# Kernel optimization log

Hardware: AMD Instinct MI355X
Metric: run time of the kernel (lower is better)

## Reference

```python
import jax, jax.numpy as jnp
import numpy as np

H = 512          # lstm_hidden_size
NUM_OPS = 8
NUM_NODES = 4
TEMP = 5.0
TANH_C = 2.5
B = 4096
NUM_STEPS = 16   # 8 lstm steps x 2 decisions (node, op)


def setup_inputs() -> dict:
    key = jax.random.key(0)
    ks = jax.random.split(key, 20)
    u = lambda k, s: jax.random.uniform(k, s, jnp.float32, -0.1, 0.1)
    inp = {}
    # embedding: torch default init N(0,1)
    inp["emb"] = jax.random.normal(ks[0], (NUM_OPS + 1, H), jnp.float32)
    # LSTM (single layer), torch gate order i,f,g,o; init U(-0.1,0.1), bias 0
    inp["w_ih"] = u(ks[1], (4 * H, H))
    inp["w_hh"] = u(ks[2], (4 * H, H))
    inp["b_ih"] = jnp.zeros((4 * H,), jnp.float32)
    inp["b_hh"] = jnp.zeros((4 * H,), jnp.float32)
    # node-predecessor decoders: widths 2,3,4,5 (one per intermediate node)
    inp["wn2"] = u(ks[3], (2, H)); inp["bn2"] = jnp.zeros((2,), jnp.float32)
    inp["wn3"] = u(ks[4], (3, H)); inp["bn3"] = jnp.zeros((3,), jnp.float32)
    inp["wn4"] = u(ks[5], (4, H)); inp["bn4"] = jnp.zeros((4,), jnp.float32)
    inp["wn5"] = u(ks[6], (5, H)); inp["bn5"] = jnp.zeros((5,), jnp.float32)
    # op decoders: one [NUM_OPS, H] decoder per intermediate node
    inp["wop"] = u(ks[7], (NUM_NODES, NUM_OPS, H))
    inp["bop"] = jnp.zeros((NUM_NODES, NUM_OPS), jnp.float32)
    # Gumbel noise for multinomial sampling via Gumbel-max (padded to width 8)
    un = jax.random.uniform(ks[8], (NUM_STEPS, B, NUM_OPS), jnp.float32,
                            minval=1e-6, maxval=1.0 - 1e-6)
    inp["gumbel"] = -jnp.log(-jnp.log(un))
    inp["batch_size"] = B
    return inp


def _lstm_step(x, h, c, w_ih, w_hh, b_ih, b_hh):
    gates = x @ w_ih.T + h @ w_hh.T + b_ih + b_hh   # [B, 4H]
    i, f, g, o = jnp.split(gates, 4, axis=-1)
    i = jax.nn.sigmoid(i); f = jax.nn.sigmoid(f)
    g = jnp.tanh(g);       o = jax.nn.sigmoid(o)
    c = f * c + i * g
    h = o * jnp.tanh(c)
    return h, c


def _decide(logits, g):
    # logits: [B, k], g: [B, k] gumbel noise -> sample ~ softmax(logits)
    logp = jax.nn.log_softmax(logits, axis=-1)
    probs = jnp.exp(logp)
    action = jnp.argmax(logits + g, axis=-1)                     # [B]
    sel = jnp.take_along_axis(logp, action[:, None], 1)[:, 0]     # [B]
    ent = -(logp * probs).sum(-1)                                 # [B]
    return action, sel, ent


def reference(emb, w_ih, w_hh, b_ih, b_hh,
              wn2, bn2, wn3, bn3, wn4, bn4, wn5, bn5,
              wop, bop, gumbel, batch_size):
    node_dec = [(wn2, bn2), (wn3, bn3), (wn4, bn4), (wn5, bn5)]
    h = jnp.zeros((batch_size, H), emb.dtype)
    c = jnp.zeros((batch_size, H), emb.dtype)
    inputs = jnp.zeros((batch_size,), jnp.int32)   # initial token 0
    actions, log_probs, entropies = [], [], []
    step = 0
    for i in range(NUM_NODES):
        wn, bn = node_dec[i]
        k = wn.shape[0]
        for _ in range(2):  # two (prev_node, op) edges per node, one lstm step each
            x = emb[inputs]                                   # [B, H]
            h, c = _lstm_step(x, h, c, w_ih, w_hh, b_ih, b_hh)
            # node-predecessor decision: temperature + tanh squashing
            nl = TANH_C * jnp.tanh((h @ wn.T + bn) / TEMP)    # [B, k]
            a, s, e = _decide(nl, gumbel[step, :, :k])
            actions.append(a); log_probs.append(s); entropies.append(e)
            step += 1
            # op decision: temperature only (no tanh in original code)
            ol = (h @ wop[i].T + bop[i]) / TEMP               # [B, NUM_OPS]
            a, s, e = _decide(ol, gumbel[step])
            actions.append(a); log_probs.append(s); entropies.append(e)
            step += 1
            inputs = a  # op action feeds the next lstm step
    return (jnp.stack(actions).astype(jnp.int32),   # [16, B]
            jnp.stack(log_probs),                   # [16, B]
            jnp.stack(entropies))                   # [16, B]
```

## Files before the change

### kernel.cpp

```cpp
#include <hip/hip_runtime.h>


constexpr int Bsz = 4096;
constexpr int Hsz = 512;
constexpr int G4H = 2048;

typedef unsigned short ushort_t;
using short8 = __attribute__((ext_vector_type(8))) short;
using f32x4 = __attribute__((ext_vector_type(4))) float;

__device__ __forceinline__ ushort_t f2bf_hi(float f) {
  unsigned u = __float_as_uint(f);
  u += 0x7FFF + ((u >> 16) & 1);
  return (ushort_t)(u >> 16);
}
__device__ __forceinline__ float bf2f(ushort_t h) {
  return __uint_as_float((unsigned)h << 16);
}
__device__ __forceinline__ float sigf(float x) {
  return 1.0f / (1.0f + expf(-x));
}

__device__ __forceinline__ void glds16(const void* gsrc, void* ldst) {
  __builtin_amdgcn_global_load_lds(
      (const __attribute__((address_space(1))) void*)gsrc,
      (__attribute__((address_space(3))) void*)ldst, 16, 0, 0);
}

__global__ __launch_bounds__(256) void setup_fused(
    const float* __restrict__ emb, const float* __restrict__ w_ih,
    const float* __restrict__ b_ih, const float* __restrict__ b_hh,
    const float* __restrict__ w_hh, float* __restrict__ Eperm,
    ushort_t* __restrict__ Wcat) {
  if (blockIdx.x < 4608) {
    const int lane = threadIdx.x & 63;
    const int wid = (blockIdx.x << 2) + (threadIdx.x >> 6);
    const int t = wid >> 11;
    const int col = wid & 2047;
    const float* er = emb + (size_t)t * Hsz + (lane << 3);
    const float* wr = w_ih + (size_t)col * Hsz + (lane << 3);
    float4 e0 = *(const float4*)(er);
    float4 e1 = *(const float4*)(er + 4);
    float4 w0 = *(const float4*)(wr);
    float4 w1 = *(const float4*)(wr + 4);
    float v = e0.x * w0.x + e0.y * w0.y + e0.z * w0.z + e0.w * w0.w +
              e1.x * w1.x + e1.y * w1.y + e1.z * w1.z + e1.w * w1.w;
#pragma unroll
    for (int off = 32; off > 0; off >>= 1) v += __shfl_xor(v, off, 64);
    if (lane == 0) {
      float val = v + b_ih[col] + b_hh[col];
      Eperm[(size_t)t * G4H + ((col & 511) << 2) + (col >> 9)] = val;
    }
  } else {
    const int b = blockIdx.x - 4608;
    const int ct = b >> 2;
    const int k = ((b & 3) << 8) + threadIdx.x;
    const int j = ct >> 2, g = ct & 3;
    const float* srcrow = w_hh + (size_t)(g * 512 + j) * Hsz;
    ushort_t out;
    if (k < 512) {
      out = f2bf_hi(srcrow[k]);
    } else {
      float x = srcrow[k - 512];
      ushort_t hi = f2bf_hi(x);
      out = f2bf_hi(x - bf2f(hi));
    }
    Wcat[(size_t)ct * 1536 + k] = out;
  }
}

template <int K>
__device__ __forceinline__ void decide_core(
    const float4 hv0, const float4 hv1, const int lane, const int r,
    const float* __restrict__ wn, const float* __restrict__ bn,
    const float* __restrict__ wopi, const float* __restrict__ bopi,
    const float* __restrict__ gum, float* __restrict__ oan,
    float* __restrict__ oao, float* __restrict__ oln, float* __restrict__ olo,
    float* __restrict__ oen, float* __restrict__ oeo,
    int* __restrict__ act_next, const int* __restrict__ cls_prev,
    int* __restrict__ cls_out) {
  float nl[K];
#pragma unroll
  for (int j = 0; j < K; ++j) {
    const float* w = wn + (size_t)j * Hsz;
    float4 w0 = *(const float4*)(w + (lane << 3));
    float4 w1 = *(const float4*)(w + (lane << 3) + 4);
    float v = hv0.x * w0.x + hv0.y * w0.y + hv0.z * w0.z + hv0.w * w0.w +
              hv1.x * w1.x + hv1.y * w1.y + hv1.z * w1.z + hv1.w * w1.w;
#pragma unroll
    for (int off = 32; off > 0; off >>= 1) v += __shfl_xor(v, off, 64);
    nl[j] = 2.5f * tanhf((v + bn[j]) / 5.0f);
  }
  float ol[8];
#pragma unroll
  for (int j = 0; j < 8; ++j) {
    const float* w = wopi + (size_t)j * Hsz;
    float4 w0 = *(const float4*)(w + (lane << 3));
    float4 w1 = *(const float4*)(w + (lane << 3) + 4);
    float v = hv0.x * w0.x + hv0.y * w0.y + hv0.z * w0.z + hv0.w * w0.w +
              hv1.x * w1.x + hv1.y * w1.y + hv1.z * w1.z + hv1.w * w1.w;
#pragma unroll
    for (int off = 32; off > 0; off >>= 1) v += __shfl_xor(v, off, 64);
    ol[j] = (v + bopi[j]) / 5.0f;
  }

  {
    const float* g = gum + (size_t)r * 8;
    float m = nl[0];
#pragma unroll
    for (int j = 1; j < K; ++j) m = fmaxf(m, nl[j]);
    float se = 0.0f;
#pragma unroll
    for (int j = 0; j < K; ++j) se += expf(nl[j] - m);
    float lse = logf(se);
    int a = 0;
    float best = nl[0] + g[0];
#pragma unroll
    for (int j = 1; j < K; ++j) {
      float v = nl[j] + g[j];
      if (v > best) { best = v; a = j; }
    }
    float ent = 0.0f, sel = 0.0f;
#pragma unroll
    for (int j = 0; j < K; ++j) {
      float lp = nl[j] - m - lse;
      ent -= lp * expf(lp);
      if (j == a) sel = lp;
    }
    if (lane == 0) { oan[r] = (float)a; oln[r] = sel; oen[r] = ent; }
  }
  {
    const float* g = gum + (size_t)Bsz * 8 + (size_t)r * 8;
    float m = ol[0];
#pragma unroll
    for (int j = 1; j < 8; ++j) m = fmaxf(m, ol[j]);
    float se = 0.0f;
#pragma unroll
    for (int j = 0; j < 8; ++j) se += expf(ol[j] - m);
    float lse = logf(se);
    int a = 0;
    float best = ol[0] + g[0];
#pragma unroll
    for (int j = 1; j < 8; ++j) {
      float v = ol[j] + g[j];
      if (v > best) { best = v; a = j; }
    }
    float ent = 0.0f, sel = 0.0f;
#pragma unroll
    for (int j = 0; j < 8; ++j) {
      float lp = ol[j] - m - lse;
      ent -= lp * expf(lp);
      if (j == a) sel = lp;
    }
    if (lane == 0) {
      oao[r] = (float)a; olo[r] = sel; oeo[r] = ent;
      act_next[r] = a;
      if (cls_out) cls_out[r] = (cls_prev ? cls_prev[r] * 8 : 0) + a;
    }
  }
}

template <int K>
__device__ __forceinline__ void decide_core_s(
    const float* __restrict__ h8, const int lane, const int r,
    const float* __restrict__ wn, const float* __restrict__ bn,
    const float* __restrict__ wopi, const float* __restrict__ bopi,
    const float* __restrict__ gum, float* __restrict__ oan,
    float* __restrict__ oao, float* __restrict__ oln, float* __restrict__ olo,
    float* __restrict__ oen, float* __restrict__ oeo,
    int* __restrict__ act_next, const int* __restrict__ cls_prev,
    int* __restrict__ cls_out) {
  float nl[K];
#pragma unroll
  for (int j = 0; j < K; ++j) {
    const float* w = wn + (size_t)j * Hsz + lane;
    float v = 0.0f;
#pragma unroll
    for (int kk = 0; kk < 8; ++kk) v = fmaf(h8[kk], w[kk * 64], v);
#pragma unroll
    for (int off = 32; off > 0; off >>= 1) v += __shfl_xor(v, off, 64);
    nl[j] = 2.5f * tanhf((v + bn[j]) / 5.0f);
  }
  float ol[8];
#pragma unroll
  for (int j = 0; j < 8; ++j) {
    const float* w = wopi + (size_t)j * Hsz + lane;
    float v = 0.0f;
#pragma unroll
    for (int kk = 0; kk < 8; ++kk) v = fmaf(h8[kk], w[kk * 64], v);
#pragma unroll
    for (int off = 32; off > 0; off >>= 1) v += __shfl_xor(v, off, 64);
    ol[j] = (v + bopi[j]) / 5.0f;
  }

  {
    const float* g = gum + (size_t)r * 8;
    float m = nl[0];
#pragma unroll
    for (int j = 1; j < K; ++j) m = fmaxf(m, nl[j]);
    float se = 0.0f;
#pragma unroll
    for (int j = 0; j < K; ++j) se += expf(nl[j] - m);
    float lse = logf(se);
    int a = 0;
    float best = nl[0] + g[0];
#pragma unroll
    for (int j = 1; j < K; ++j) {
      float v = nl[j] + g[j];
      if (v > best) { best = v; a = j; }
    }
    float ent = 0.0f, sel = 0.0f;
#pragma unroll
    for (int j = 0; j < K; ++j) {
      float lp = nl[j] - m - lse;
      ent -= lp * expf(lp);
      if (j == a) sel = lp;
    }
    if (lane == 0) { oan[r] = (float)a; oln[r] = sel; oen[r] = ent; }
  }
  {
    const float* g = gum + (size_t)Bsz * 8 + (size_t)r * 8;
    float m = ol[0];
#pragma unroll
    for (int j = 1; j < 8; ++j) m = fmaxf(m, ol[j]);
    float se = 0.0f;
#pragma unroll
    for (int j = 0; j < 8; ++j) se += expf(ol[j] - m);
    float lse = logf(se);
    int a = 0;
    float best = ol[0] + g[0];
#pragma unroll
    for (int j = 1; j < 8; ++j) {
      float v = ol[j] + g[j];
      if (v > best) { best = v; a = j; }
    }
    float ent = 0.0f, sel = 0.0f;
#pragma unroll
    for (int j = 0; j < 8; ++j) {
      float lp = ol[j] - m - lse;
      ent -= lp * expf(lp);
      if (j == a) sel = lp;
    }
    if (lane == 0) {
      oao[r] = (float)a; olo[r] = sel; oeo[r] = ent;
      act_next[r] = a;
      if (cls_out) cls_out[r] = (cls_prev ? cls_prev[r] * 8 : 0) + a;
    }
  }
}

template <int K>
__global__ __launch_bounds__(256) void decide_step(
    const float* __restrict__ h, const float* __restrict__ wn,
    const float* __restrict__ bn, const float* __restrict__ wopi,
    const float* __restrict__ bopi, const float* __restrict__ gum,
    float* __restrict__ oan, float* __restrict__ oao,
    float* __restrict__ oln, float* __restrict__ olo,
    float* __restrict__ oen, float* __restrict__ oeo,
    int* __restrict__ act_next, const int* __restrict__ hidx, int hmode,
    const int* __restrict__ cls_prev, int* __restrict__ cls_out) {
  const int lane = threadIdx.x & 63;
  const int r = (blockIdx.x << 2) + (threadIdx.x >> 6);
  const int idx = (hmode == 1) ? r : hidx[r];
  const float* hr = h + (size_t)idx * Hsz;
  const float4 hv0 = *(const float4*)(hr + (lane << 3));
  const float4 hv1 = *(const float4*)(hr + (lane << 3) + 4);
  decide_core<K>(hv0, hv1, lane, r, wn, bn, wopi, bopi, gum, oan, oao, oln,
                 olo, oen, oeo, act_next, cls_prev, cls_out);
}

__global__ __launch_bounds__(256) void decide0_step(
    const float* __restrict__ Eperm, const float* __restrict__ wn,
    const float* __restrict__ bn, const float* __restrict__ wopi,
    const float* __restrict__ bopi, const float* __restrict__ gum,
    float* __restrict__ oan, float* __restrict__ oao,
    float* __restrict__ oln, float* __restrict__ olo,
    float* __restrict__ oen, float* __restrict__ oeo,
    int* __restrict__ act_next, int* __restrict__ cls_out) {
  const int lane = threadIdx.x & 63;
  const int r = (blockIdx.x << 2) + (threadIdx.x >> 6);
  float h8[8];
#pragma unroll
  for (int kk = 0; kk < 8; ++kk) {
    float4 e = *(const float4*)&Eperm[(size_t)(((lane << 3) + kk) << 2)];
    float ig = sigf(e.x);
    float gg = tanhf(e.z);
    float og = sigf(e.w);
    float cn = ig * gg;
    h8[kk] = og * tanhf(cn);
  }
  float4 hv0 = {h8[0], h8[1], h8[2], h8[3]};
  float4 hv1 = {h8[4], h8[5], h8[6], h8[7]};
  decide_core<2>(hv0, hv1, lane, r, wn, bn, wopi, bopi, gum, oan, oao, oln,
                 olo, oen, oeo, act_next, nullptr, cls_out);
}

__global__ __launch_bounds__(256) void fused_step1(
    const float* __restrict__ Eperm, const float* __restrict__ w_hh,
    float* __restrict__ h2, float* __restrict__ c2) {
  const int lane = threadIdx.x & 63;
  const int j = (blockIdx.x << 2) + (threadIdx.x >> 6);
  float h8[8];
#pragma unroll
  for (int kk = 0; kk < 8; ++kk) {
    float4 e = *(const float4*)&Eperm[(size_t)(((lane << 3) + kk) << 2)];
    h8[kk] = sigf(e.w) * tanhf(sigf(e.x) * tanhf(e.z));
  }
  float v[4];
#pragma unroll
  for (int g = 0; g < 4; ++g) {
    const float* w = w_hh + (size_t)(g * 512 + j) * Hsz + (lane << 3);
    float4 w0 = *(const float4*)(w);
    float4 w1 = *(const float4*)(w + 4);
    v[g] = h8[0] * w0.x + h8[1] * w0.y + h8[2] * w0.z + h8[3] * w0.w +
           h8[4] * w1.x + h8[5] * w1.y + h8[6] * w1.z + h8[7] * w1.w;
  }
#pragma unroll
  for (int off = 32; off > 0; off >>= 1) {
#pragma unroll
    for (int g = 0; g < 4; ++g) v[g] += __shfl_xor(v[g], off, 64);
  }
  float4 e0 = *(const float4*)&Eperm[(size_t)(j << 2)];
  float c1j = sigf(e0.x) * tanhf(e0.z);
  if (lane < 8) {
    const int er = lane;
    float4 e = *(const float4*)&Eperm[(size_t)er * G4H + (j << 2)];
    float ig = sigf(v[0] + e.x);
    float fg = sigf(v[1] + e.y);
    float gg = tanhf(v[2] + e.z);
    float og = sigf(v[3] + e.w);
    float cn = fg * c1j + ig * gg;
    h2[er * Hsz + j] = og * tanhf(cn);
    c2[er * Hsz + j] = cn;
  }
}

__global__ __launch_bounds__(256) void fused_step2(
    const float* __restrict__ Eperm, const float* __restrict__ w_hh,
    const float* __restrict__ h2, const float* __restrict__ c2,
    float* __restrict__ h3, float* __restrict__ c3) {
  const int lane = threadIdx.x & 63;
  const int wid = (blockIdx.x << 2) + (threadIdx.x >> 6);
  const int gq = wid >> 9, j = wid & 511;
  const float* hr = h2 + (size_t)gq * Hsz + (lane << 3);
  float4 a0 = *(const float4*)(hr);
  float4 a1 = *(const float4*)(hr + 4);
  float v[4];
#pragma unroll
  for (int g = 0; g < 4; ++g) {
    const float* w = w_hh + (size_t)(g * 512 + j) * Hsz + (lane << 3);
    float4 w0 = *(const float4*)(w);
    float4 w1 = *(const float4*)(w + 4);
    v[g] = a0.x * w0.x + a0.y * w0.y + a0.z * w0.z + a0.w * w0.w +
           a1.x * w1.x + a1.y * w1.y + a1.z * w1.z + a1.w * w1.w;
  }
#pragma unroll
  for (int off = 32; off > 0; off >>= 1) {
#pragma unroll
    for (int g = 0; g < 4; ++g) v[g] += __shfl_xor(v[g], off, 64);
  }
  float cp = c2[(size_t)gq * Hsz + j];
  if (lane < 8) {
    const int er = lane;
    float4 e = *(const float4*)&Eperm[(size_t)er * G4H + (j << 2)];
    float ig = sigf(v[0] + e.x);
    float fg = sigf(v[1] + e.y);
    float gg = tanhf(v[2] + e.z);
    float og = sigf(v[3] + e.w);
    float cn = fg * cp + ig * gg;
    h3[(size_t)((gq << 3) + er) * Hsz + j] = og * tanhf(cn);
    c3[(size_t)((gq << 3) + er) * Hsz + j] = cn;
  }
}

template <int NRT, int SK>
__global__ __launch_bounds__(256) void gemm64ct_sk(
    const float* __restrict__ A, const float* __restrict__ w_hh,
    float* __restrict__ Gpart) {
  constexpr int LOG = (NRT == 1) ? 0 : (NRT == 2) ? 1 : (NRT == 4) ? 2 : 3;
  constexpr int LDA = 68;
  __shared__ float As[16 * LDA];
  __shared__ float Bs[16 * LDA];
  const int tid = threadIdx.x;
  const int bx = blockIdx.x & 31;
  const int by = (blockIdx.x >> 5) & (NRT - 1);
  const int s = blockIdx.x >> (5 + LOG);
  const int r0 = by * 64, c0 = bx * 64;
  const int tx = tid & 15, ty = tid >> 4;
  const int lr = tid >> 2;
  const int lk = (tid & 3) << 2;
  const int ct = c0 + lr;
  const int brow = (ct & 3) * 512 + (ct >> 2);
  const float* Ar = A + (size_t)(r0 + lr) * Hsz;
  const float* Br = w_hh + (size_t)brow * Hsz;
  float acc[4][4];
#pragma unroll
  for (int i = 0; i < 4; ++i)
#pragma unroll
    for (int j = 0; j < 4; ++j) acc[i][j] = 0.0f;

  const int kBeg = s * (Hsz / SK);
  const int kEnd = kBeg + Hsz / SK;
  for (int k0 = kBeg; k0 < kEnd; k0 += 16) {
    float4 a = *(const float4*)(Ar + k0 + lk);
    float4 b = *(const float4*)(Br + k0 + lk);
    __syncthreads();
    As[(lk + 0) * LDA + lr] = a.x;
    As[(lk + 1) * LDA + lr] = a.y;
    As[(lk + 2) * LDA + lr] = a.z;
    As[(lk + 3) * LDA + lr] = a.w;
    Bs[(lk + 0) * LDA + lr] = b.x;
    Bs[(lk + 1) * LDA + lr] = b.y;
    Bs[(lk + 2) * LDA + lr] = b.z;
    Bs[(lk + 3) * LDA + lr] = b.w;
    __syncthreads();
#pragma unroll
    for (int kk = 0; kk < 16; ++kk) {
      float4 av = *(const float4*)&As[kk * LDA + (ty << 2)];
      float4 bv = *(const float4*)&Bs[kk * LDA + (tx << 2)];
      float avs[4] = {av.x, av.y, av.z, av.w};
      float bvs[4] = {bv.x, bv.y, bv.z, bv.w};
#pragma unroll
      for (int i = 0; i < 4; ++i)
#pragma unroll
        for (int j = 0; j < 4; ++j) acc[i][j] = fmaf(avs[i], bvs[j], acc[i][j]);
    }
  }
  const int jcol = (c0 >> 2) + tx;
#pragma unroll
  for (int i = 0; i < 4; ++i) {
    float4 o = {acc[i][0], acc[i][1], acc[i][2], acc[i][3]};
    *(float4*)&Gpart[((size_t)(s * NRT * 64) + r0 + (ty << 2) + i) * G4H +
                     (jcol << 2)] = o;
  }
}

__global__ __launch_bounds__(256) void fused_step3red(
    const float* __restrict__ Gpart, const float* __restrict__ Eperm,
    const float* __restrict__ c3, float* __restrict__ h4,
    float* __restrict__ c4) {
  const int idx = blockIdx.x * 256 + threadIdx.x;
  const int q = idx >> 9, j = idx & 511;
  float4 g = {0.f, 0.f, 0.f, 0.f};
#pragma unroll
  for (int s = 0; s < 8; ++s) {
    float4 p = *(const float4*)&Gpart[(size_t)(s * 64 + q) * G4H + (j << 2)];
    g.x += p.x; g.y += p.y; g.z += p.z; g.w += p.w;
  }
  const float cp = c3[(size_t)q * Hsz + j];
#pragma unroll
  for (int er = 0; er < 8; ++er) {
    float4 e = *(const float4*)&Eperm[(size_t)er * G4H + (j << 2)];
    float ig = sigf(g.x + e.x);
    float fg = sigf(g.y + e.y);
    float gg = tanhf(g.z + e.z);
    float og = sigf(g.w + e.w);
    float cn = fg * cp + ig * gg;
    h4[(size_t)((q << 3) + er) * Hsz + j] = og * tanhf(cn);
    c4[(size_t)((q << 3) + er) * Hsz + j] = cn;
  }
}

__global__ __launch_bounds__(256) void decide4_fused(
    const float* __restrict__ Gperm, const float* __restrict__ Gperm2,
    const float* __restrict__ Eperm, const float* __restrict__ c4,
    const int* __restrict__ cls, float* __restrict__ cF,
    ushort_t* __restrict__ Acat, const float* __restrict__ wn,
    const float* __restrict__ bn, const float* __restrict__ wopi,
    const float* __restrict__ bopi, const float* __restrict__ gum,
    float* __restrict__ oan, float* __restrict__ oao,
    float* __restrict__ oln, float* __restrict__ olo,
    float* __restrict__ oen, float* __restrict__ oeo,
    int* __restrict__ act) {
  const int lane = threadIdx.x & 63;
  const int r = (blockIdx.x << 2) + (threadIdx.x >> 6);
  const int q = cls[r];
  const int er = act[r];
  const float* Gr = Gperm + (size_t)q * G4H;
  const float* Gr2 = Gperm2 + (size_t)q * G4H;
  const float* Er = Eperm + (size_t)er * G4H;
  float h8[8];
#pragma unroll
  for (int kk = 0; kk < 8; ++kk) {
    const int j = kk * 64 + lane;
    float4 g4 = *(const float4*)&Gr[j << 2];
    float4 p4 = *(const float4*)&Gr2[j << 2];
    float4 e4 = *(const float4*)&Er[j << 2];
    float ig = sigf(g4.x + p4.x + e4.x);
    float fg = sigf(g4.y + p4.y + e4.y);
    float gg = tanhf(g4.z + p4.z + e4.z);
    float og = sigf(g4.w + p4.w + e4.w);
    float cn = fg * c4[(size_t)q * Hsz + j] + ig * gg;
    float hn = og * tanhf(cn);
    cF[(size_t)r * Hsz + j] = cn;
    h8[kk] = hn;
    ushort_t hi = f2bf_hi(hn);
    Acat[(size_t)r * 1024 + j] = hi;
    Acat[(size_t)r * 1024 + 512 + j] = f2bf_hi(hn - bf2f(hi));
  }
  decide_core_s<4>(h8, lane, r, wn, bn, wopi, bopi, gum, oan, oao, oln,
                   olo, oen, oeo, act, nullptr, nullptr);
}

__global__ __launch_bounds__(256) void gemm_bf16_lstm(
    const ushort_t* __restrict__ Acat, const ushort_t* __restrict__ Wcat,
    const float* __restrict__ Eperm, const int* __restrict__ act,
    float* __restrict__ cF, float* __restrict__ h_out,
    ushort_t* __restrict__ Aout) {
  __shared__ union {
    ushort_t P[2][4][128 * 32];
    float C[64 * 132];
  } sm;

  const int tid = threadIdx.x;
  const int wave = tid >> 6, lane = tid & 63;
  const int xcd = blockIdx.x & 7;
  const int i64 = blockIdx.x >> 3;
  const int by = ((xcd >> 1) << 3) + (i64 >> 3);
  const int bx = ((xcd & 1) << 3) + (i64 & 7);
  const int r0 = by * 128, c0 = bx * 128;
  const int wr = (wave >> 1) * 64, wc = (wave & 1) * 64;
  const int mrow = lane & 15, quad = lane >> 4;

  const int srow = lane >> 2;
  const int sk = (lane & 3) << 3;

  const ushort_t* sbase[8];
  int doff[8];
#pragma unroll
  for (int q = 0; q < 8; ++q) {
    const int g = (q << 2) + wave;
    const int panel = g >> 3;
    const int region = g & 7;
    const int row = region * 16 + srow;
    if (panel == 0)
      sbase[q] = Acat + (size_t)(r0 + row) * 1024 + sk;
    else if (panel == 1)
      sbase[q] = Acat + (size_t)(r0 + row) * 1024 + 512 + sk;
    else if (panel == 2)
      sbase[q] = Wcat + (size_t)(c0 + row) * 1536 + sk;
    else
      sbase[q] = Wcat + (size_t)(c0 + row) * 1536 + 512 + sk;
    doff[q] = panel * 8192 + region * 1024;
  }

  f32x4 acc[4][4];
#pragma unroll
  for (int i = 0; i < 4; ++i)
#pragma unroll
    for (int jt = 0; jt < 4; ++jt) acc[i][jt] = (f32x4){0.f, 0.f, 0.f, 0.f};

  auto stage = [&](int buf, int it) {
    const int ks = it << 5;
#pragma unroll
    for (int q = 0; q < 8; ++q)
      glds16(sbase[q] + ks, (char*)sm.P[0][0] + (buf << 15) + doff[q]);
  };

  stage(0, 0);
  __syncthreads();

  int cur = 0;
  for (int it = 0; it < 16; ++it) {
    if (it < 15) stage(cur ^ 1, it + 1);
    const ushort_t* AH = sm.P[cur][0];
    const ushort_t* AL = sm.P[cur][1];
    const ushort_t* BH = sm.P[cur][2];
    const ushort_t* BL = sm.P[cur][3];
    short8 ah[4], al[4], bh[4], bl[4];
#pragma unroll
    for (int i = 0; i < 4; ++i) {
      ah[i] = *(const short8*)&AH[(wr + i * 16 + mrow) * 32 + (quad << 3)];
      al[i] = *(const short8*)&AL[(wr + i * 16 + mrow) * 32 + (quad << 3)];
    }
#pragma unroll
    for (int jt = 0; jt < 4; ++jt) {
      bh[jt] = *(const short8*)&BH[(wc + jt * 16 + mrow) * 32 + (quad << 3)];
      bl[jt] = *(const short8*)&BL[(wc + jt * 16 + mrow) * 32 + (quad << 3)];
    }
#pragma unroll
    for (int i = 0; i < 4; ++i)
#pragma unroll
      for (int jt = 0; jt < 4; ++jt) {
        acc[i][jt] = __builtin_amdgcn_mfma_f32_16x16x32_bf16(
            ah[i], bh[jt], acc[i][jt], 0, 0, 0);
        acc[i][jt] = __builtin_amdgcn_mfma_f32_16x16x32_bf16(
            ah[i], bl[jt], acc[i][jt], 0, 0, 0);
        acc[i][jt] = __builtin_amdgcn_mfma_f32_16x16x32_bf16(
            al[i], bh[jt], acc[i][jt], 0, 0, 0);
      }
    __syncthreads();
    cur ^= 1;
  }

  const int jj = tid & 31;
  const int rbase = tid >> 5;
#pragma unroll
  for (int p = 0; p < 2; ++p) {
    __syncthreads();
    if ((wr >> 6) == p) {
#pragma unroll
      for (int i = 0; i < 4; ++i)
#pragma unroll
        for (int jt = 0; jt < 4; ++jt)
#pragma unroll
          for (int rg = 0; rg < 4; ++rg)
            sm.C[(i * 16 + quad * 4 + rg) * 132 + wc + jt * 16 + mrow] =
                acc[i][jt][rg];
    }
    __syncthreads();
#pragma unroll
    for (int rp = 0; rp < 8; ++rp) {
      const int rl = rbase * 8 + rp;
      const int grow = r0 + p * 64 + rl;
      float4 g4 = *(float4*)&sm.C[rl * 132 + jj * 4];
      const int a = act[grow];
      const int jglob = (c0 >> 2) + jj;
      float4 e4 = *(const float4*)&Eperm[(size_t)a * G4H + c0 + jj * 4];
      float iv = g4.x + e4.x, fv = g4.y + e4.y;
      float gv = g4.z + e4.z, ov = g4.w + e4.w;
      float ig = 1.0f / (1.0f + expf(-iv));
      float fg = 1.0f / (1.0f + expf(-fv));
      float gg = tanhf(gv);
      float og = 1.0f / (1.0f + expf(-ov));
      const size_t ci = (size_t)grow * Hsz + jglob;
      float cn = fg * cF[ci] + ig * gg;
      float hn = og * tanhf(cn);
      cF[ci] = cn;
      h_out[ci] = hn;
      ushort_t hi = f2bf_hi(hn);
      Aout[(size_t)grow * 1024 + jglob] = hi;
      Aout[(size_t)grow * 1024 + 512 + jglob] = f2bf_hi(hn - bf2f(hi));
    }
  }
}

extern "C" void kernel_launch(void* const* d_in, const int* in_sizes, int n_in,
                              void* d_out, int out_size, void* d_ws,
                              size_t ws_size, hipStream_t stream) {
  (void)in_sizes; (void)n_in; (void)out_size; (void)ws_size;
  const float* emb = (const float*)d_in[0];
  const float* w_ih = (const float*)d_in[1];
  const float* w_hh = (const float*)d_in[2];
  const float* b_ih = (const float*)d_in[3];
  const float* b_hh = (const float*)d_in[4];
  const float* wn[4] = {(const float*)d_in[5], (const float*)d_in[7],
                        (const float*)d_in[9], (const float*)d_in[11]};
  const float* bn[4] = {(const float*)d_in[6], (const float*)d_in[8],
                        (const float*)d_in[10], (const float*)d_in[12]};
  const float* wop = (const float*)d_in[13];
  const float* bop = (const float*)d_in[14];
  const float* gum = (const float*)d_in[15];

  float* ws = (float*)d_ws;
  float* Eperm = ws;             ws += 9 * G4H;
  float* h2 = ws;                ws += 8 * Hsz;
  float* c2 = ws;                ws += 8 * Hsz;
  float* h3 = ws;                ws += 64 * Hsz;
  float* c3 = ws;                ws += 64 * Hsz;
  float* h4 = ws;                ws += 512 * Hsz;
  float* c4 = ws;                ws += 512 * Hsz;
  float* Gperm = ws;
  ushort_t* AcatB = (ushort_t*)Gperm;
  ws += (8u << 20) / 4;
  ushort_t* AcatA = (ushort_t*)ws;      ws += (8u << 20) / 4;
  ushort_t* Wcat = (ushort_t*)ws;       ws += (6u << 20) / 4;
  float* hA = ws;                ws += (size_t)Bsz * Hsz;
  float* cF = ws;                ws += (size_t)Bsz * Hsz;
  int* act = (int*)ws;
  int* cls = act + Bsz;

  float* out = (float*)d_out;
  const size_t SZ = (size_t)16 * Bsz;

  auto outp = [&](int s, float*& oan, float*& oao, float*& oln, float*& olo,
                  float*& oen, float*& oeo, const float*& gn) {
    oan = out + (size_t)(2 * s) * Bsz;
    oao = out + (size_t)(2 * s + 1) * Bsz;
    oln = out + SZ + (size_t)(2 * s) * Bsz;
    olo = out + SZ + (size_t)(2 * s + 1) * Bsz;
    oen = out + 2 * SZ + (size_t)(2 * s) * Bsz;
    oeo = out + 2 * SZ + (size_t)(2 * s + 1) * Bsz;
    gn = gum + (size_t)(2 * s) * Bsz * 8;
  };

  auto decide = [&](int s, const float* h, int hmode, const int* hidx,
                    const int* cls_prev, int* cls_out) {
    const int i = s >> 1;
    float *oan, *oao, *oln, *olo, *oen, *oeo;
    const float* gn;
    outp(s, oan, oao, oln, olo, oen, oeo, gn);
    const float* wopi = wop + (size_t)i * 8 * Hsz;
    const float* bopi = bop + (size_t)i * 8;
    switch (i) {
      case 0:
        decide_step<2><<<Bsz / 4, 256, 0, stream>>>(h, wn[0], bn[0], wopi, bopi,
            gn, oan, oao, oln, olo, oen, oeo, act, hidx, hmode, cls_prev, cls_out);
        break;
      case 1:
        decide_step<3><<<Bsz / 4, 256, 0, stream>>>(h, wn[1], bn[1], wopi, bopi,
            gn, oan, oao, oln, olo, oen, oeo, act, hidx, hmode, cls_prev, cls_out);
        break;
      case 2:
        decide_step<4><<<Bsz / 4, 256, 0, stream>>>(h, wn[2], bn[2], wopi, bopi,
            gn, oan, oao, oln, olo, oen, oeo, act, hidx, hmode, cls_prev, cls_out);
        break;
      default:
        decide_step<5><<<Bsz / 4, 256, 0, stream>>>(h, wn[3], bn[3], wopi, bopi,
            gn, oan, oao, oln, olo, oen, oeo, act, hidx, hmode, cls_prev, cls_out);
        break;
    }
  };

  setup_fused<<<4608 + 8192, 256, 0, stream>>>(emb, w_ih, b_ih, b_hh, w_hh,
                                               Eperm, Wcat);

  {
    float *oan, *oao, *oln, *olo, *oen, *oeo;
    const float* gn;
    outp(0, oan, oao, oln, olo, oen, oeo, gn);
    decide0_step<<<Bsz / 4, 256, 0, stream>>>(Eperm, wn[0], bn[0], wop, bop,
        gn, oan, oao, oln, olo, oen, oeo, act, cls);
  }

  fused_step1<<<128, 256, 0, stream>>>(Eperm, w_hh, h2, c2);
  decide(1, h2, 2, cls, cls, cls);

  fused_step2<<<1024, 256, 0, stream>>>(Eperm, w_hh, h2, c2, h3, c3);
  decide(2, h3, 2, cls, cls, cls);

  gemm64ct_sk<1, 8><<<32 * 8, 256, 0, stream>>>(h3, w_hh, Gperm);
  fused_step3red<<<128, 256, 0, stream>>>(Gperm, Eperm, c3, h4, c4);
  decide(3, h4, 2, cls, nullptr, nullptr);

  gemm64ct_sk<8, 2><<<32 * 8 * 2, 256, 0, stream>>>(h4, w_hh, Gperm);
  {
    float *oan, *oao, *oln, *olo, *oen, *oeo;
    const float* gn;
    outp(4, oan, oao, oln, olo, oen, oeo, gn);
    decide4_fused<<<Bsz / 4, 256, 0, stream>>>(Gperm,
        Gperm + (size_t)512 * G4H, Eperm, c4, cls, cF, AcatA, wn[2], bn[2],
        wop + (size_t)2 * 8 * Hsz, bop + 2 * 8, gn,
        oan, oao, oln, olo, oen, oeo, act);
  }

  ushort_t* ain = AcatA;
  ushort_t* aout = AcatB;
  for (int s = 5; s < 8; ++s) {
    gemm_bf16_lstm<<<512, 256, 0, stream>>>(ain, Wcat, Eperm, act, cF, hA, aout);
    decide(s, hA, 1, nullptr, nullptr, nullptr);
    ushort_t* t = ain; ain = aout; aout = t;
  }
}
```

Baseline: 375.4 us.

## Load A fragments directly from global into registers, stage only B in LDS

The LSTM GEMM kernel now reads the A operand (hi/lo bf16 hidden state) straight from global memory into register fragments with double-buffered registers. Only the weight panels are staged through LDS, which halves the LDS footprint and allows launch_bounds with 2 blocks per SM. The aim is to cut LDS traffic and raise occupancy. In exchange, A loads are uncoalesced-ish per-lane global reads, and both waves sharing a row band now load the same A rows redundantly.

```diff
diff --git a/kernel.cpp b/kernel.cpp
--- a/kernel.cpp
+++ b/kernel.cpp
@@ -502,13 +502,13 @@
                    olo, oen, oeo, act, nullptr, nullptr);
 }
 
-__global__ __launch_bounds__(256) void gemm_bf16_lstm(
+__global__ __launch_bounds__(256, 2) void gemm_bf16_lstm(
     const ushort_t* __restrict__ Acat, const ushort_t* __restrict__ Wcat,
     const float* __restrict__ Eperm, const int* __restrict__ act,
     float* __restrict__ cF, float* __restrict__ h_out,
     ushort_t* __restrict__ Aout) {
   __shared__ union {
-    ushort_t P[2][4][128 * 32];
+    ushort_t B[2][2][128 * 32];
     float C[64 * 132];
   } sm;
 
@@ -524,25 +524,22 @@
 
   const int srow = lane >> 2;
   const int sk = (lane & 3) << 3;
-
-  const ushort_t* sbase[8];
-  int doff[8];
-#pragma unroll
-  for (int q = 0; q < 8; ++q) {
+  const ushort_t* sbase[4];
+  int doff[4];
+#pragma unroll
+  for (int q = 0; q < 4; ++q) {
     const int g = (q << 2) + wave;
-    const int panel = g >> 3;
+    const int half = g >> 3;
     const int region = g & 7;
     const int row = region * 16 + srow;
-    if (panel == 0)
-      sbase[q] = Acat + (size_t)(r0 + row) * 1024 + sk;
-    else if (panel == 1)
-      sbase[q] = Acat + (size_t)(r0 + row) * 1024 + 512 + sk;
-    else if (panel == 2)
-      sbase[q] = Wcat + (size_t)(c0 + row) * 1536 + sk;
-    else
-      sbase[q] = Wcat + (size_t)(c0 + row) * 1536 + 512 + sk;
-    doff[q] = panel * 8192 + region * 1024;
-  }
+    sbase[q] = Wcat + (size_t)(c0 + row) * 1536 + half * 512 + sk;
+    doff[q] = half * 8192 + region * 1024;
+  }
+
+  const ushort_t* aRow[4];
+#pragma unroll
+  for (int i = 0; i < 4; ++i)
+    aRow[i] = Acat + (size_t)(r0 + wr + i * 16 + mrow) * 1024 + (quad << 3);
 
   f32x4 acc[4][4];
 #pragma unroll
@@ -550,33 +547,27 @@
 #pragma unroll
     for (int jt = 0; jt < 4; ++jt) acc[i][jt] = (f32x4){0.f, 0.f, 0.f, 0.f};
 
-  auto stage = [&](int buf, int it) {
+  auto stageB = [&](int buf, int it) {
     const int ks = it << 5;
 #pragma unroll
-    for (int q = 0; q < 8; ++q)
-      glds16(sbase[q] + ks, (char*)sm.P[0][0] + (buf << 15) + doff[q]);
+    for (int q = 0; q < 4; ++q)
+      glds16(sbase[q] + ks, (char*)sm.B[buf][0] + doff[q]);
   };
-
-  stage(0, 0);
-  __syncthreads();
-
-  int cur = 0;
-  for (int it = 0; it < 16; ++it) {
-    if (it < 15) stage(cur ^ 1, it + 1);
-    const ushort_t* AH = sm.P[cur][0];
-    const ushort_t* AL = sm.P[cur][1];
-    const ushort_t* BH = sm.P[cur][2];
-    const ushort_t* BL = sm.P[cur][3];
-    short8 ah[4], al[4], bh[4], bl[4];
+  auto loadA = [&](short8* ah, short8* al, int it) {
+    const int ks = it << 5;
 #pragma unroll
     for (int i = 0; i < 4; ++i) {
-      ah[i] = *(const short8*)&AH[(wr + i * 16 + mrow) * 32 + (quad << 3)];
-      al[i] = *(const short8*)&AL[(wr + i * 16 + mrow) * 32 + (quad << 3)];
-    }
+      ah[i] = *(const short8*)(aRow[i] + ks);
+      al[i] = *(const short8*)(aRow[i] + 512 + ks);
+    }
+  };
+  auto compute = [&](const short8* ah, const short8* al, int buf) {
+    short8 bh[4], bl[4];
 #pragma unroll
     for (int jt = 0; jt < 4; ++jt) {
-      bh[jt] = *(const short8*)&BH[(wc + jt * 16 + mrow) * 32 + (quad << 3)];
-      bl[jt] = *(const short8*)&BL[(wc + jt * 16 + mrow) * 32 + (quad << 3)];
+      const int off = (wc + jt * 16 + mrow) * 32 + (quad << 3);
+      bh[jt] = *(const short8*)&sm.B[buf][0][off];
+      bl[jt] = *(const short8*)&sm.B[buf][1][off];
     }
 #pragma unroll
     for (int i = 0; i < 4; ++i)
@@ -589,8 +580,25 @@
         acc[i][jt] = __builtin_amdgcn_mfma_f32_16x16x32_bf16(
             al[i], bh[jt], acc[i][jt], 0, 0, 0);
       }
+  };
+
+  short8 ah0[4], al0[4], ah1[4], al1[4];
+  loadA(ah0, al0, 0);
+  stageB(0, 0);
+  __syncthreads();
+
+  for (int it2 = 0; it2 < 8; ++it2) {
+    const int it = it2 << 1;
+    loadA(ah1, al1, it + 1);
+    stageB(1, it + 1);
+    compute(ah0, al0, 0);
     __syncthreads();
-    cur ^= 1;
+    if (it + 2 < 16) {
+      loadA(ah0, al0, it + 2);
+      stageB(0, it + 2);
+    }
+    compute(ah1, al1, 1);
+    __syncthreads();
   }
 
   const int jj = tid & 31;
```

New measurement: 439.1 us. +17.0%, slower.
